# Optimization experiments

Measured on AMD Instinct MI355X. Metric: run time of the kernel, lower is better.

The kernel has to match this reference:

```python
import jax, jax.numpy as jnp
import numpy as np

N_EMBED = 768
N_HEAD = 12
HEAD = N_EMBED // N_HEAD
B, T = 4, 2048


def setup_inputs() -> dict:
    key = jax.random.key(0)
    ks = jax.random.split(key, 12)
    s = 0.02
    d = N_EMBED
    return {
        "x": jax.random.normal(ks[0], (B, T, d), jnp.float32),
        "ln1_g": jnp.ones((d,), jnp.float32),
        "ln1_b": jnp.zeros((d,), jnp.float32),
        "w_attn": jax.random.normal(ks[1], (d, 3 * d), jnp.float32) * s,
        "b_attn": jnp.zeros((3 * d,), jnp.float32),
        "w_aproj": jax.random.normal(ks[2], (d, d), jnp.float32) * s,
        "b_aproj": jnp.zeros((d,), jnp.float32),
        "ln2_g": jnp.ones((d,), jnp.float32),
        "ln2_b": jnp.zeros((d,), jnp.float32),
        "w_fc": jax.random.normal(ks[3], (d, 4 * d), jnp.float32) * s,
        "b_fc": jnp.zeros((4 * d,), jnp.float32),
        "w_mproj": jax.random.normal(ks[4], (4 * d, d), jnp.float32) * s,
        "b_mproj": jnp.zeros((d,), jnp.float32),
    }


def _layernorm(x, g, b, eps=1e-5):
    mu = jnp.mean(x, axis=-1, keepdims=True)
    var = jnp.var(x, axis=-1, keepdims=True)
    return (x - mu) * jax.lax.rsqrt(var + eps) * g + b


def _attn(x, w_attn, b_attn, w_aproj, b_aproj):
    Bq, Tq, C = x.shape
    qkv = x @ w_attn + b_attn  # [B,T,3C]
    q, k, v = jnp.split(qkv, 3, axis=2)
    q = q.reshape(Bq, Tq, N_HEAD, HEAD).transpose(0, 2, 1, 3)  # [B,H,T,hd]
    k = k.reshape(Bq, Tq, N_HEAD, HEAD).transpose(0, 2, 1, 3)
    v = v.reshape(Bq, Tq, N_HEAD, HEAD).transpose(0, 2, 1, 3)
    att = jnp.einsum("bhqd,bhkd->bhqk", q, k) * (1.0 / np.sqrt(HEAD))
    causal = jnp.tril(jnp.ones((Tq, Tq), bool))
    att = jnp.where(causal, att, -jnp.inf)
    att = jax.nn.softmax(att, axis=-1)
    y = jnp.einsum("bhqk,bhkd->bhqd", att, v)
    y = y.transpose(0, 2, 1, 3).reshape(Bq, Tq, C)
    return y @ w_aproj + b_aproj


def reference(x, ln1_g, ln1_b, w_attn, b_attn, w_aproj, b_aproj,
              ln2_g, ln2_b, w_fc, b_fc, w_mproj, b_mproj):
    x = x + _attn(_layernorm(x, ln1_g, ln1_b), w_attn, b_attn, w_aproj, b_aproj)
    h = _layernorm(x, ln2_g, ln2_b)
    h = jax.nn.gelu(h @ w_fc + b_fc, approximate=False)
    x = x + (h @ w_mproj + b_mproj)
    return x
```

## Files before the change

### kernel.cpp

```cpp
#include <hip/hip_runtime.h>
#include <hip/hip_bf16.h>

#define NE 768
#define NH 12
#define HD 64
#define BB 4
#define TT 2048
#define ROWS (BB*TT)

typedef __attribute__((ext_vector_type(8))) short bf16x8;
typedef __attribute__((ext_vector_type(4))) float f32x4;

__device__ __forceinline__ short f2bf(float f) {
  __hip_bfloat16 h = __float2bfloat16(f);
  union { __hip_bfloat16 h; short s; } u; u.h = h; return u.s;
}

__device__ __forceinline__ void gload16(const void* g, void* l) {
  __builtin_amdgcn_global_load_lds(
      (const __attribute__((address_space(1))) void*)g,
      (__attribute__((address_space(3))) void*)l,
      16, 0, 0);
}

__global__ __launch_bounds__(256) void wtrans_kernel(
    const float* __restrict__ W, short* __restrict__ Wt, int K, int N) {
  __shared__ short tile[64 * 65];
  int k0 = blockIdx.x * 64, n0 = blockIdx.y * 64;
  int t = threadIdx.x;
#pragma unroll
  for (int p = 0; p < 16; ++p) {
    int idx = p * 256 + t;
    int r = idx >> 6, c = idx & 63;
    tile[r * 65 + c] = f2bf(W[(size_t)(k0 + r) * N + n0 + c]);
  }
  __syncthreads();
#pragma unroll
  for (int p = 0; p < 16; ++p) {
    int idx = p * 256 + t;
    int rr = idx >> 6, cc = idx & 63;
    Wt[(size_t)(n0 + rr) * K + k0 + cc] = tile[cc * 65 + rr];
  }
}

__global__ __launch_bounds__(256) void vtrans_kernel(
    const short* __restrict__ qkv, short* __restrict__ vt) {
  __shared__ short tile[64 * 65];
  int bh = blockIdx.x;
  int b = bh / NH, h = bh % NH;
  int t0 = blockIdx.y * 64;
  int t = threadIdx.x;
#pragma unroll
  for (int p = 0; p < 16; ++p) {
    int idx = p * 256 + t;
    int r = idx >> 6, c = idx & 63;
    tile[r * 65 + c] =
        qkv[(size_t)(b * TT + t0 + r) * (3 * NE) + 2 * NE + h * HD + c];
  }
  __syncthreads();
#pragma unroll
  for (int p = 0; p < 16; ++p) {
    int idx = p * 256 + t;
    int rr = idx >> 6, cc = idx & 63;
    vt[(size_t)bh * HD * TT + (size_t)rr * TT + t0 + cc] = tile[cc * 65 + rr];
  }
}

__global__ __launch_bounds__(64) void ln_kernel(
    const float* __restrict__ x, const float* __restrict__ g,
    const float* __restrict__ b, short* __restrict__ out) {
  int row = blockIdx.x, l = threadIdx.x;
  const float* xr = x + (size_t)row * NE;
  float4 v[3];
  float s = 0.f, ss = 0.f;
#pragma unroll
  for (int i = 0; i < 3; ++i) {
    v[i] = *reinterpret_cast<const float4*>(xr + l * 4 + i * 256);
    s += v[i].x + v[i].y + v[i].z + v[i].w;
    ss += v[i].x * v[i].x + v[i].y * v[i].y + v[i].z * v[i].z + v[i].w * v[i].w;
  }
#pragma unroll
  for (int m = 1; m < 64; m <<= 1) {
    s += __shfl_xor(s, m);
    ss += __shfl_xor(ss, m);
  }
  float mu = s * (1.0f / NE);
  float var = ss * (1.0f / NE) - mu * mu;
  float rstd = rsqrtf(var + 1e-5f);
#pragma unroll
  for (int i = 0; i < 3; ++i) {
    float4 gv = *reinterpret_cast<const float4*>(g + l * 4 + i * 256);
    float4 bv = *reinterpret_cast<const float4*>(b + l * 4 + i * 256);
    short4 o;
    o.x = f2bf((v[i].x - mu) * rstd * gv.x + bv.x);
    o.y = f2bf((v[i].y - mu) * rstd * gv.y + bv.y);
    o.z = f2bf((v[i].z - mu) * rstd * gv.z + bv.z);
    o.w = f2bf((v[i].w - mu) * rstd * gv.w + bv.w);
    *reinterpret_cast<short4*>(out + (size_t)row * NE + l * 4 + i * 256) = o;
  }
}

template <int EPI>
__global__ __launch_bounds__(256) void gemm_kernel(
    const short* __restrict__ A, const short* __restrict__ Bt,
    const float* __restrict__ bias, const float* __restrict__ resid,
    void* __restrict__ Cout, int M, int N, int K) {
  __shared__ short As[128 * 64];
  __shared__ short Bs[128 * 64];
  int t = threadIdx.x;
  int w = t >> 6, l = t & 63;
  int wr = w >> 1, wc = w & 1;
  int bn = blockIdx.x, bm = blockIdx.y;
  int lr = l & 15, lkb = (l >> 4) * 8;

  f32x4 acc[4][4];
#pragma unroll
  for (int i = 0; i < 4; ++i)
#pragma unroll
    for (int j = 0; j < 4; ++j) acc[i][j] = (f32x4){0.f, 0.f, 0.f, 0.f};

  const short* ga = A + (size_t)(bm * 128 + (t >> 3)) * K + (t & 7) * 8;
  const short* gb = Bt + (size_t)(bn * 128 + (t >> 3)) * K + (t & 7) * 8;
  short* lA = As + t * 8;
  short* lB = Bs + t * 8;
  int nk = K >> 6;
  for (int kt = 0; kt < nk; ++kt) {
    __syncthreads();
#pragma unroll
    for (int p = 0; p < 4; ++p) {
      gload16(ga + (size_t)(p * 32) * K, lA + p * 2048);
      gload16(gb + (size_t)(p * 32) * K, lB + p * 2048);
    }
    ga += 64; gb += 64;
    __syncthreads();
#pragma unroll
    for (int kc = 0; kc < 2; ++kc) {
      bf16x8 af[4], bfr[4];
#pragma unroll
      for (int i = 0; i < 4; ++i)
        af[i] = *reinterpret_cast<const bf16x8*>(
            As + (wr * 64 + i * 16 + lr) * 64 + kc * 32 + lkb);
#pragma unroll
      for (int j = 0; j < 4; ++j)
        bfr[j] = *reinterpret_cast<const bf16x8*>(
            Bs + (wc * 64 + j * 16 + lr) * 64 + kc * 32 + lkb);
#pragma unroll
      for (int i = 0; i < 4; ++i)
#pragma unroll
        for (int j = 0; j < 4; ++j)
          acc[i][j] = __builtin_amdgcn_mfma_f32_16x16x32_bf16(af[i], bfr[j], acc[i][j], 0, 0, 0);
    }
  }

  int rbase = bm * 128 + wr * 64;
  int cbase = bn * 128 + wc * 64;
#pragma unroll
  for (int i = 0; i < 4; ++i) {
#pragma unroll
    for (int r = 0; r < 4; ++r) {
      int row = rbase + i * 16 + (l >> 4) * 4 + r;
#pragma unroll
      for (int j = 0; j < 4; ++j) {
        int col = cbase + j * 16 + lr;
        float v = acc[i][j][r] + bias[col];
        if (EPI == 0) {
          ((short*)Cout)[(size_t)row * N + col] = f2bf(v);
        } else if (EPI == 1) {
          v = 0.5f * v * (1.0f + erff(v * 0.70710678118654752f));
          ((short*)Cout)[(size_t)row * N + col] = f2bf(v);
        } else {
          ((float*)Cout)[(size_t)row * N + col] = v + resid[(size_t)row * N + col];
        }
      }
    }
  }
}

template <int EPI>
__global__ __launch_bounds__(256) void gemm64_kernel(
    const short* __restrict__ A, const short* __restrict__ Bt,
    const float* __restrict__ bias, const float* __restrict__ resid,
    void* __restrict__ Cout, int M, int N, int K) {
  __shared__ short As[128 * 64];
  __shared__ short Bs[64 * 64];
  int t = threadIdx.x;
  int w = t >> 6, l = t & 63;
  int bn = blockIdx.x, bm = blockIdx.y;
  int lr = l & 15, lkb = (l >> 4) * 8;

  f32x4 acc[2][4];
#pragma unroll
  for (int i = 0; i < 2; ++i)
#pragma unroll
    for (int j = 0; j < 4; ++j) acc[i][j] = (f32x4){0.f, 0.f, 0.f, 0.f};

  const short* ga = A + (size_t)(bm * 128 + (t >> 3)) * K + (t & 7) * 8;
  const short* gb = Bt + (size_t)(bn * 64 + (t >> 3)) * K + (t & 7) * 8;
  short* lA = As + t * 8;
  short* lB = Bs + t * 8;
  int nk = K >> 6;
  for (int kt = 0; kt < nk; ++kt) {
    __syncthreads();
#pragma unroll
    for (int p = 0; p < 4; ++p)
      gload16(ga + (size_t)(p * 32) * K, lA + p * 2048);
#pragma unroll
    for (int p = 0; p < 2; ++p)
      gload16(gb + (size_t)(p * 32) * K, lB + p * 2048);
    ga += 64; gb += 64;
    __syncthreads();
#pragma unroll
    for (int kc = 0; kc < 2; ++kc) {
      bf16x8 af[2], bfr[4];
#pragma unroll
      for (int i = 0; i < 2; ++i)
        af[i] = *reinterpret_cast<const bf16x8*>(
            As + (w * 32 + i * 16 + lr) * 64 + kc * 32 + lkb);
#pragma unroll
      for (int j = 0; j < 4; ++j)
        bfr[j] = *reinterpret_cast<const bf16x8*>(
            Bs + (j * 16 + lr) * 64 + kc * 32 + lkb);
#pragma unroll
      for (int i = 0; i < 2; ++i)
#pragma unroll
        for (int j = 0; j < 4; ++j)
          acc[i][j] = __builtin_amdgcn_mfma_f32_16x16x32_bf16(af[i], bfr[j], acc[i][j], 0, 0, 0);
    }
  }

  int rbase = bm * 128 + w * 32;
  int cbase = bn * 64;
#pragma unroll
  for (int i = 0; i < 2; ++i) {
#pragma unroll
    for (int r = 0; r < 4; ++r) {
      int row = rbase + i * 16 + (l >> 4) * 4 + r;
#pragma unroll
      for (int j = 0; j < 4; ++j) {
        int col = cbase + j * 16 + lr;
        float v = acc[i][j][r] + bias[col];
        if (EPI == 0) {
          ((short*)Cout)[(size_t)row * N + col] = f2bf(v);
        } else if (EPI == 1) {
          v = 0.5f * v * (1.0f + erff(v * 0.70710678118654752f));
          ((short*)Cout)[(size_t)row * N + col] = f2bf(v);
        } else {
          ((float*)Cout)[(size_t)row * N + col] = v + resid[(size_t)row * N + col];
        }
      }
    }
  }
}

__global__ __launch_bounds__(256, 4) void attn_kernel(
    const short* __restrict__ qkv, const short* __restrict__ vt,
    short* __restrict__ y) {
  __shared__ short Ks[2][64 * 64];
  __shared__ short Vs[2][64 * 64];
  int t = threadIdx.x, w = t >> 6, l = t & 63;
  int lr = l & 15, g = l >> 4, lkb = g * 8;
  int bh = blockIdx.x;
  int b = bh / NH, h = bh % NH;
  int qt = ((int)gridDim.y - 1) - blockIdx.y;
  int qbase = qt * 64;
  const int rstride = 3 * NE;

  const short* qrow = qkv + (size_t)(b * TT + qbase + w * 16 + lr) * rstride + h * HD + lkb;
  bf16x8 qf0 = *reinterpret_cast<const bf16x8*>(qrow);
  bf16x8 qf1 = *reinterpret_cast<const bf16x8*>(qrow + 32);

  f32x4 o[4];
#pragma unroll
  for (int j = 0; j < 4; ++j) o[j] = (f32x4){0.f, 0.f, 0.f, 0.f};
  float m_run = -3e38f, l_run = 0.f;

  int ci0 = t, ci1 = t + 256;
  int row0 = ci0 >> 3, c0 = ((ci0 & 7) ^ (row0 & 7)) * 8;
  int row1 = ci1 >> 3, c1 = ((ci1 & 7) ^ (row1 & 7)) * 8;

  const short* kbase = qkv + (size_t)(b * TT) * rstride + NE + h * HD;
  const short* vtb = vt + (size_t)bh * HD * TT;

  gload16(kbase + (size_t)row0 * rstride + c0, &Ks[0][ci0 * 8]);
  gload16(kbase + (size_t)row1 * rstride + c1, &Ks[0][ci1 * 8]);
  gload16(vtb + (size_t)row0 * TT + c0, &Vs[0][ci0 * 8]);
  gload16(vtb + (size_t)row1 * TT + c1, &Vs[0][ci1 * 8]);

  int qmin = qbase + w * 16;
  int srcA = ((g & 1) * 2) * 16 + lr;
  int srcB = srcA + 16;
  bool ghi = (g >= 2);

  int nkv = qt + 1;
  for (int kt = 0; kt < nkv; ++kt) {
    int bi = kt & 1;
    int kvbase = kt * 64;
    bool pre = (kt + 1 < nkv);
    __syncthreads();

    if (pre) {
      int nb = kvbase + 64;
      gload16(kbase + (size_t)(nb + row0) * rstride + c0, &Ks[bi ^ 1][ci0 * 8]);
      gload16(kbase + (size_t)(nb + row1) * rstride + c1, &Ks[bi ^ 1][ci1 * 8]);
      gload16(vtb + (size_t)row0 * TT + nb + c0, &Vs[bi ^ 1][ci0 * 8]);
      gload16(vtb + (size_t)row1 * TT + nb + c1, &Vs[bi ^ 1][ci1 * 8]);
    }

    f32x4 s[4];
#pragma unroll
    for (int nt = 0; nt < 4; ++nt) {
      int row = nt * 16 + lr;
      bf16x8 kf0 = *reinterpret_cast<const bf16x8*>(
          (char*)Ks[bi] + ((row * 128 + lkb * 2) ^ ((lr & 7) << 4)));
      bf16x8 kf1 = *reinterpret_cast<const bf16x8*>(
          (char*)Ks[bi] + ((row * 128 + 64 + lkb * 2) ^ ((lr & 7) << 4)));
      f32x4 st = (f32x4){0.f, 0.f, 0.f, 0.f};
      st = __builtin_amdgcn_mfma_f32_16x16x32_bf16(kf0, qf0, st, 0, 0, 0);
      st = __builtin_amdgcn_mfma_f32_16x16x32_bf16(kf1, qf1, st, 0, 0, 0);
      s[nt] = st;
    }

    if (kvbase + 63 > qmin) {
      int qabs = qmin + lr;
#pragma unroll
      for (int nt = 0; nt < 4; ++nt)
#pragma unroll
        for (int r = 0; r < 4; ++r) {
          int kp = kvbase + nt * 16 + g * 4 + r;
          s[nt][r] = (kp <= qabs) ? s[nt][r] * 0.125f : -3e38f;
        }
    } else {
#pragma unroll
      for (int nt = 0; nt < 4; ++nt)
#pragma unroll
        for (int r = 0; r < 4; ++r)
          s[nt][r] *= 0.125f;
    }

    float mx = s[0][0];
#pragma unroll
    for (int nt = 0; nt < 4; ++nt)
#pragma unroll
      for (int r = 0; r < 4; ++r) mx = fmaxf(mx, s[nt][r]);
    mx = fmaxf(mx, __shfl_xor(mx, 16));
    mx = fmaxf(mx, __shfl_xor(mx, 32));
    if (__any(mx > m_run + 8.f)) {
      float mn = fmaxf(m_run, mx);
      float al = __expf(m_run - mn);
      m_run = mn;
      l_run *= al;
      float al0 = __shfl(al, g * 4 + 0);
      float al1 = __shfl(al, g * 4 + 1);
      float al2 = __shfl(al, g * 4 + 2);
      float al3 = __shfl(al, g * 4 + 3);
#pragma unroll
      for (int j = 0; j < 4; ++j) {
        o[j][0] *= al0; o[j][1] *= al1; o[j][2] *= al2; o[j][3] *= al3;
      }
    }
    float rs = 0.f;
#pragma unroll
    for (int nt = 0; nt < 4; ++nt)
#pragma unroll
      for (int r = 0; r < 4; ++r) {
        float p = __expf(s[nt][r] - m_run);
        s[nt][r] = p;
        rs += p;
      }
    rs += __shfl_xor(rs, 16);
    rs += __shfl_xor(rs, 32);
    l_run += rs;

    unsigned int pw[4][2];
#pragma unroll
    for (int nt = 0; nt < 4; ++nt)
#pragma unroll
      for (int pr = 0; pr < 2; ++pr)
        pw[nt][pr] = (unsigned int)(unsigned short)f2bf(s[nt][2 * pr]) |
                     ((unsigned int)(unsigned short)f2bf(s[nt][2 * pr + 1]) << 16);

#pragma unroll
    for (int c = 0; c < 2; ++c) {
      unsigned int a00 = __shfl(pw[c * 2 + 0][0], srcA);
      unsigned int a01 = __shfl(pw[c * 2 + 0][1], srcA);
      unsigned int a02 = __shfl(pw[c * 2 + 0][0], srcB);
      unsigned int a03 = __shfl(pw[c * 2 + 0][1], srcB);
      unsigned int a10 = __shfl(pw[c * 2 + 1][0], srcA);
      unsigned int a11 = __shfl(pw[c * 2 + 1][1], srcA);
      unsigned int a12 = __shfl(pw[c * 2 + 1][0], srcB);
      unsigned int a13 = __shfl(pw[c * 2 + 1][1], srcB);
      unsigned int u0 = ghi ? a10 : a00;
      unsigned int u1 = ghi ? a11 : a01;
      unsigned int u2 = ghi ? a12 : a02;
      unsigned int u3 = ghi ? a13 : a03;
      bf16x8 pa;
      pa[0] = (short)(u0 & 0xffffu); pa[1] = (short)(u0 >> 16);
      pa[2] = (short)(u1 & 0xffffu); pa[3] = (short)(u1 >> 16);
      pa[4] = (short)(u2 & 0xffffu); pa[5] = (short)(u2 >> 16);
      pa[6] = (short)(u3 & 0xffffu); pa[7] = (short)(u3 >> 16);
#pragma unroll
      for (int j = 0; j < 4; ++j) {
        int vrow = j * 16 + lr;
        bf16x8 vf = *reinterpret_cast<const bf16x8*>(
            (char*)Vs[bi] + ((vrow * 128 + c * 64 + lkb * 2) ^ ((lr & 7) << 4)));
        o[j] = __builtin_amdgcn_mfma_f32_16x16x32_bf16(pa, vf, o[j], 0, 0, 0);
      }
    }
  }

  float inv = 1.0f / l_run;
  float i0 = __shfl(inv, g * 4 + 0);
  float i1 = __shfl(inv, g * 4 + 1);
  float i2 = __shfl(inv, g * 4 + 2);
  float i3 = __shfl(inv, g * 4 + 3);
#pragma unroll
  for (int r = 0; r < 4; ++r) {
    float ir = (r == 0) ? i0 : (r == 1) ? i1 : (r == 2) ? i2 : i3;
    size_t row = (size_t)(b * TT + qbase + w * 16 + g * 4 + r);
#pragma unroll
    for (int j = 0; j < 4; ++j)
      y[row * NE + h * HD + j * 16 + lr] = f2bf(o[j][r] * ir);
  }
}

extern "C" void kernel_launch(void* const* d_in, const int* in_sizes, int n_in,
                              void* d_out, int out_size, void* d_ws, size_t ws_size,
                              hipStream_t stream) {
  (void)in_sizes; (void)n_in; (void)out_size; (void)ws_size;
  const float* x       = (const float*)d_in[0];
  const float* ln1_g   = (const float*)d_in[1];
  const float* ln1_b   = (const float*)d_in[2];
  const float* w_attn  = (const float*)d_in[3];
  const float* b_attn  = (const float*)d_in[4];
  const float* w_aproj = (const float*)d_in[5];
  const float* b_aproj = (const float*)d_in[6];
  const float* ln2_g   = (const float*)d_in[7];
  const float* ln2_b   = (const float*)d_in[8];
  const float* w_fc    = (const float*)d_in[9];
  const float* b_fc    = (const float*)d_in[10];
  const float* w_mproj = (const float*)d_in[11];
  const float* b_mproj = (const float*)d_in[12];

  char* ws = (char*)d_ws;
  size_t off = 0;
  auto alloc = [&](size_t bytes) {
    char* p = ws + off;
    off += (bytes + 255) & ~(size_t)255;
    return p;
  };
  short* wt_attn  = (short*)alloc((size_t)2304 * 768 * 2);
  short* wt_aproj = (short*)alloc((size_t)768 * 768 * 2);
  short* wt_fc    = (short*)alloc((size_t)3072 * 768 * 2);
  short* wt_mproj = (short*)alloc((size_t)768 * 3072 * 2);
  short* lnb  = (short*)alloc((size_t)ROWS * 768 * 2);
  short* qkvb = (short*)alloc((size_t)ROWS * 3072 * 2);
  short* yb   = (short*)alloc((size_t)ROWS * 768 * 2);
  float* x2   = (float*)alloc((size_t)ROWS * 768 * 4);
  short* vtg = lnb;

  wtrans_kernel<<<dim3(768 / 64, 2304 / 64), 256, 0, stream>>>(w_attn, wt_attn, 768, 2304);
  wtrans_kernel<<<dim3(768 / 64, 768 / 64), 256, 0, stream>>>(w_aproj, wt_aproj, 768, 768);
  wtrans_kernel<<<dim3(768 / 64, 3072 / 64), 256, 0, stream>>>(w_fc, wt_fc, 768, 3072);
  wtrans_kernel<<<dim3(3072 / 64, 768 / 64), 256, 0, stream>>>(w_mproj, wt_mproj, 3072, 768);

  ln_kernel<<<ROWS, 64, 0, stream>>>(x, ln1_g, ln1_b, lnb);
  gemm_kernel<0><<<dim3(2304 / 128, ROWS / 128), 256, 0, stream>>>(
      lnb, wt_attn, b_attn, nullptr, qkvb, ROWS, 2304, 768);
  vtrans_kernel<<<dim3(BB * NH, TT / 64), 256, 0, stream>>>(qkvb, vtg);
  attn_kernel<<<dim3(BB * NH, TT / 64), 256, 0, stream>>>(qkvb, vtg, yb);
  gemm64_kernel<2><<<dim3(768 / 64, ROWS / 128), 256, 0, stream>>>(
      yb, wt_aproj, b_aproj, x, x2, ROWS, 768, 768);
  ln_kernel<<<ROWS, 64, 0, stream>>>(x2, ln2_g, ln2_b, lnb);
  gemm_kernel<1><<<dim3(3072 / 128, ROWS / 128), 256, 0, stream>>>(
      lnb, wt_fc, b_fc, nullptr, qkvb, ROWS, 3072, 768);
  gemm64_kernel<2><<<dim3(768 / 64, ROWS / 128), 256, 0, stream>>>(
      qkvb, wt_mproj, b_mproj, x2, (float*)d_out, ROWS, 768, 3072);
}
```

Baseline: 343.1 us.

## Double-buffer GEMM LDS tiles with XOR-swizzled layout and prefetch

Both GEMM kernels now keep two LDS buffers holding K-slices of 32 and prefetch the next slice with direct global-to-LDS loads while MFMAs run on the current one. This replaces the load/sync/compute pattern that had two barriers per step with one barrier per step. The loads also XOR-swizzle 16-byte chunks by row so the fragment reads avoid LDS bank conflicts. The trade-offs are more loop iterations with less MFMA work per barrier, and a reliance on the single barrier per iteration being enough to order the async LDS writes.

```diff
diff --git a/kernel.cpp b/kernel.cpp
--- a/kernel.cpp
+++ b/kernel.cpp
@@ -105,13 +105,13 @@
     const short* __restrict__ A, const short* __restrict__ Bt,
     const float* __restrict__ bias, const float* __restrict__ resid,
     void* __restrict__ Cout, int M, int N, int K) {
-  __shared__ short As[128 * 64];
-  __shared__ short Bs[128 * 64];
+  __shared__ short As[2][128 * 32];
+  __shared__ short Bs[2][128 * 32];
   int t = threadIdx.x;
   int w = t >> 6, l = t & 63;
   int wr = w >> 1, wc = w & 1;
   int bn = blockIdx.x, bm = blockIdx.y;
-  int lr = l & 15, lkb = (l >> 4) * 8;
+  int lr = l & 15, g4 = l >> 4;
 
   f32x4 acc[4][4];
 #pragma unroll
@@ -119,37 +119,44 @@
 #pragma unroll
     for (int j = 0; j < 4; ++j) acc[i][j] = (f32x4){0.f, 0.f, 0.f, 0.f};
 
-  const short* ga = A + (size_t)(bm * 128 + (t >> 3)) * K + (t & 7) * 8;
-  const short* gb = Bt + (size_t)(bn * 128 + (t >> 3)) * K + (t & 7) * 8;
-  short* lA = As + t * 8;
-  short* lB = Bs + t * 8;
-  int nk = K >> 6;
+  int r0 = t >> 2;
+  int cs = ((t & 3) ^ (r0 & 3)) * 8;
+  const short* ga = A + (size_t)(bm * 128) * K;
+  const short* gb = Bt + (size_t)(bn * 128) * K;
+
+  gload16(ga + (size_t)r0 * K + cs, &As[0][t * 8]);
+  gload16(ga + (size_t)(r0 + 64) * K + cs, &As[0][(t + 256) * 8]);
+  gload16(gb + (size_t)r0 * K + cs, &Bs[0][t * 8]);
+  gload16(gb + (size_t)(r0 + 64) * K + cs, &Bs[0][(t + 256) * 8]);
+
+  int xorA = (lr & 3) << 4;
+  int nk = K >> 5;
   for (int kt = 0; kt < nk; ++kt) {
+    int bi = kt & 1;
     __syncthreads();
-#pragma unroll
-    for (int p = 0; p < 4; ++p) {
-      gload16(ga + (size_t)(p * 32) * K, lA + p * 2048);
-      gload16(gb + (size_t)(p * 32) * K, lB + p * 2048);
-    }
-    ga += 64; gb += 64;
-    __syncthreads();
-#pragma unroll
-    for (int kc = 0; kc < 2; ++kc) {
-      bf16x8 af[4], bfr[4];
-#pragma unroll
-      for (int i = 0; i < 4; ++i)
-        af[i] = *reinterpret_cast<const bf16x8*>(
-            As + (wr * 64 + i * 16 + lr) * 64 + kc * 32 + lkb);
+    if (kt + 1 < nk) {
+      int ko = (kt + 1) * 32;
+      gload16(ga + (size_t)r0 * K + ko + cs, &As[bi ^ 1][t * 8]);
+      gload16(ga + (size_t)(r0 + 64) * K + ko + cs, &As[bi ^ 1][(t + 256) * 8]);
+      gload16(gb + (size_t)r0 * K + ko + cs, &Bs[bi ^ 1][t * 8]);
+      gload16(gb + (size_t)(r0 + 64) * K + ko + cs, &Bs[bi ^ 1][(t + 256) * 8]);
+    }
+    const char* Ab = (const char*)As[bi];
+    const char* Bb = (const char*)Bs[bi];
+    bf16x8 af[4], bfr[4];
+#pragma unroll
+    for (int i = 0; i < 4; ++i)
+      af[i] = *reinterpret_cast<const bf16x8*>(
+          Ab + (((wr * 64 + i * 16 + lr) * 64 + g4 * 16) ^ xorA));
+#pragma unroll
+    for (int j = 0; j < 4; ++j)
+      bfr[j] = *reinterpret_cast<const bf16x8*>(
+          Bb + (((wc * 64 + j * 16 + lr) * 64 + g4 * 16) ^ xorA));
+#pragma unroll
+    for (int i = 0; i < 4; ++i)
 #pragma unroll
       for (int j = 0; j < 4; ++j)
-        bfr[j] = *reinterpret_cast<const bf16x8*>(
-            Bs + (wc * 64 + j * 16 + lr) * 64 + kc * 32 + lkb);
-#pragma unroll
-      for (int i = 0; i < 4; ++i)
-#pragma unroll
-        for (int j = 0; j < 4; ++j)
-          acc[i][j] = __builtin_amdgcn_mfma_f32_16x16x32_bf16(af[i], bfr[j], acc[i][j], 0, 0, 0);
-    }
+        acc[i][j] = __builtin_amdgcn_mfma_f32_16x16x32_bf16(af[i], bfr[j], acc[i][j], 0, 0, 0);
   }
 
   int rbase = bm * 128 + wr * 64;
@@ -158,7 +165,7 @@
   for (int i = 0; i < 4; ++i) {
 #pragma unroll
     for (int r = 0; r < 4; ++r) {
-      int row = rbase + i * 16 + (l >> 4) * 4 + r;
+      int row = rbase + i * 16 + g4 * 4 + r;
 #pragma unroll
       for (int j = 0; j < 4; ++j) {
         int col = cbase + j * 16 + lr;
@@ -181,12 +188,12 @@
     const short* __restrict__ A, const short* __restrict__ Bt,
     const float* __restrict__ bias, const float* __restrict__ resid,
     void* __restrict__ Cout, int M, int N, int K) {
-  __shared__ short As[128 * 64];
-  __shared__ short Bs[64 * 64];
+  __shared__ short As[2][128 * 32];
+  __shared__ short Bs[2][64 * 32];
   int t = threadIdx.x;
   int w = t >> 6, l = t & 63;
   int bn = blockIdx.x, bm = blockIdx.y;
-  int lr = l & 15, lkb = (l >> 4) * 8;
+  int lr = l & 15, g4 = l >> 4;
 
   f32x4 acc[2][4];
 #pragma unroll
@@ -194,38 +201,42 @@
 #pragma unroll
     for (int j = 0; j < 4; ++j) acc[i][j] = (f32x4){0.f, 0.f, 0.f, 0.f};
 
-  const short* ga = A + (size_t)(bm * 128 + (t >> 3)) * K + (t & 7) * 8;
-  const short* gb = Bt + (size_t)(bn * 64 + (t >> 3)) * K + (t & 7) * 8;
-  short* lA = As + t * 8;
-  short* lB = Bs + t * 8;
-  int nk = K >> 6;
+  int r0 = t >> 2;
+  int cs = ((t & 3) ^ (r0 & 3)) * 8;
+  const short* ga = A + (size_t)(bm * 128) * K;
+  const short* gb = Bt + (size_t)(bn * 64) * K;
+
+  gload16(ga + (size_t)r0 * K + cs, &As[0][t * 8]);
+  gload16(ga + (size_t)(r0 + 64) * K + cs, &As[0][(t + 256) * 8]);
+  gload16(gb + (size_t)r0 * K + cs, &Bs[0][t * 8]);
+
+  int xorA = (lr & 3) << 4;
+  int nk = K >> 5;
   for (int kt = 0; kt < nk; ++kt) {
+    int bi = kt & 1;
     __syncthreads();
-#pragma unroll
-    for (int p = 0; p < 4; ++p)
-      gload16(ga + (size_t)(p * 32) * K, lA + p * 2048);
-#pragma unroll
-    for (int p = 0; p < 2; ++p)
-      gload16(gb + (size_t)(p * 32) * K, lB + p * 2048);
-    ga += 64; gb += 64;
-    __syncthreads();
-#pragma unroll
-    for (int kc = 0; kc < 2; ++kc) {
-      bf16x8 af[2], bfr[4];
-#pragma unroll
-      for (int i = 0; i < 2; ++i)
-        af[i] = *reinterpret_cast<const bf16x8*>(
-            As + (w * 32 + i * 16 + lr) * 64 + kc * 32 + lkb);
+    if (kt + 1 < nk) {
+      int ko = (kt + 1) * 32;
+      gload16(ga + (size_t)r0 * K + ko + cs, &As[bi ^ 1][t * 8]);
+      gload16(ga + (size_t)(r0 + 64) * K + ko + cs, &As[bi ^ 1][(t + 256) * 8]);
+      gload16(gb + (size_t)r0 * K + ko + cs, &Bs[bi ^ 1][t * 8]);
+    }
+    const char* Ab = (const char*)As[bi];
+    const char* Bb = (const char*)Bs[bi];
+    bf16x8 af[2], bfr[4];
+#pragma unroll
+    for (int i = 0; i < 2; ++i)
+      af[i] = *reinterpret_cast<const bf16x8*>(
+          Ab + (((w * 32 + i * 16 + lr) * 64 + g4 * 16) ^ xorA));
+#pragma unroll
+    for (int j = 0; j < 4; ++j)
+      bfr[j] = *reinterpret_cast<const bf16x8*>(
+          Bb + (((j * 16 + lr) * 64 + g4 * 16) ^ xorA));
+#pragma unroll
+    for (int i = 0; i < 2; ++i)
 #pragma unroll
       for (int j = 0; j < 4; ++j)
-        bfr[j] = *reinterpret_cast<const bf16x8*>(
-            Bs + (j * 16 + lr) * 64 + kc * 32 + lkb);
-#pragma unroll
-      for (int i = 0; i < 2; ++i)
-#pragma unroll
-        for (int j = 0; j < 4; ++j)
-          acc[i][j] = __builtin_amdgcn_mfma_f32_16x16x32_bf16(af[i], bfr[j], acc[i][j], 0, 0, 0);
-    }
+        acc[i][j] = __builtin_amdgcn_mfma_f32_16x16x32_bf16(af[i], bfr[j], acc[i][j], 0, 0, 0);
   }
 
   int rbase = bm * 128 + w * 32;
@@ -234,7 +245,7 @@
   for (int i = 0; i < 2; ++i) {
 #pragma unroll
     for (int r = 0; r < 4; ++r) {
-      int row = rbase + i * 16 + (l >> 4) * 4 + r;
+      int row = rbase + i * 16 + g4 * 4 + r;
 #pragma unroll
       for (int j = 0; j < 4; ++j) {
         int col = cbase + j * 16 + lr;
```

New measurement: 318.6 us. 7.1% less time.
